# Kernel tuning notes

Measured on AMD Instinct MI355X. Metric: run time of the kernel, lower is better.

## Reference

```python
import jax, jax.numpy as jnp
import numpy as np

BS, C, H, W = 128, 256, 9, 9
D = 9                      # spectral window size
PS = 15                    # padsize
PAD_SPACE = PS - H         # 6
PAD1 = D // 2              # 4 (spectral pad)
START = PAD_SPACE // 2     # 3 (output crop offset)
SPE_HEAD = 25
SHARE_HEAD = 9
SIDE = 5                   # spe_head_Sidelength
BN_EPS = 1e-5


def setup_inputs() -> dict:
    key = jax.random.key(0)
    ks = jax.random.split(key, 12)
    s = 0.1
    return {
        "x": jax.random.normal(ks[0], (BS, C, H, W), jnp.float32),
        "wk": jax.random.normal(ks[1], (H * W, 1, D), jnp.float32) * s,   # depthwise conv1d over spectral axis
        "bk": jax.random.normal(ks[2], (H * W,), jnp.float32) * s,
        "w1": jax.random.normal(ks[3], (SPE_HEAD, SHARE_HEAD, 2 * SHARE_HEAD), jnp.float32) * s,  # grouped 1x1, no bias
        "bn_gamma": jnp.ones((SPE_HEAD * SHARE_HEAD,), jnp.float32),
        "bn_beta": jnp.zeros((SPE_HEAD * SHARE_HEAD,), jnp.float32),
        "bn_mean": jax.random.normal(ks[4], (SPE_HEAD * SHARE_HEAD,), jnp.float32) * s,
        "bn_var": jax.random.uniform(ks[5], (SPE_HEAD * SHARE_HEAD,), jnp.float32, 0.5, 1.5),
        "w2": jax.random.normal(ks[6], (SPE_HEAD, D, SHARE_HEAD), jnp.float32) * s,  # grouped 1x1 -> spe_head*d
        "b2": jax.random.normal(ks[7], (SPE_HEAD * D,), jnp.float32) * s,
        "wv": jax.random.normal(ks[8], (C, 1, 3, 3), jnp.float32) * s,   # depthwise 3x3
        "bv": jax.random.normal(ks[9], (C,), jnp.float32) * s,
    }


def _unfold_k3_d5(t, bs, c):
    # torch nn.Unfold(kernel=3, dilation=5) on a 15x15 map -> 5x5 output positions.
    # row = kh*5 + oh, col = kw*5 + ow, so a plain (3,5,3,5) reshape gives the taps.
    t = t.reshape(bs, c, 3, SIDE, 3, SIDE)              # (bs,c,kh,oh,kw,ow)
    t = t.transpose(0, 1, 2, 4, 3, 5)                   # (bs,c,kh,kw,oh,ow)
    t = t.reshape(bs, c * SHARE_HEAD, SPE_HEAD)          # (bs, c*9, 25) torch unfold layout
    return t.transpose(0, 2, 1)                          # (bs, 25, c*9)


def reference(x, wk, bk, w1, bn_gamma, bn_beta, bn_mean, bn_var, w2, b2, wv, bv):
    bs, c, h, w = x.shape
    # --- key: depthwise conv1d along spectral (channel) axis, one filter per pixel ---
    k = x.reshape(bs, c, h * w).transpose(0, 2, 1)       # (bs, 81, c)
    k1 = jax.lax.conv_general_dilated(
        k, wk, (1,), [(PAD1, PAD1)],
        dimension_numbers=("NCH", "OIH", "NCH"), feature_group_count=h * w,
    ) + bk[None, :, None]                                # (bs, 81, c)
    k1 = k1.transpose(0, 2, 1).reshape(bs, c, h, w)

    # --- pad right/bottom and unfold q, k ---
    k1_pad = jnp.pad(k1, ((0, 0), (0, 0), (0, PAD_SPACE), (0, PAD_SPACE)))  # (bs,c,15,15)
    q_pad = jnp.pad(x, ((0, 0), (0, 0), (0, PAD_SPACE), (0, PAD_SPACE)))
    key_u = _unfold_k3_d5(k1_pad, bs, c)                 # (bs,25,9c)
    q_u = _unfold_k3_d5(q_pad, bs, c)

    # stack + reshape exactly as torch (row-major): (bs,25,2,9c) -> (bs,450,c)
    key_q = jnp.stack((q_u, key_u), axis=2).reshape(bs, 2 * SPE_HEAD * SHARE_HEAD, c)

    # --- attention_embed: grouped 1x1 conv -> BN(eval) -> ReLU -> grouped 1x1 conv ---
    a = jnp.einsum("goi,bgic->bgoc", w1, key_q.reshape(bs, SPE_HEAD, 2 * SHARE_HEAD, c))
    a = a.reshape(bs, SPE_HEAD * SHARE_HEAD, c)          # (bs,225,c)
    inv_std = bn_gamma / jnp.sqrt(bn_var + BN_EPS)
    a = (a - bn_mean[None, :, None]) * inv_std[None, :, None] + bn_beta[None, :, None]
    a = jax.nn.relu(a)
    a = jnp.einsum("goi,bgic->bgoc", w2, a.reshape(bs, SPE_HEAD, SHARE_HEAD, c))
    a = a.reshape(bs, SPE_HEAD * D, c) + b2[None, :, None]  # (bs,225,c)

    # --- build per-pixel spectral kernels: tile, rearrange to 15x15, softmax over d ---
    att = jnp.tile(a.reshape(bs, SPE_HEAD, D, c), (1, SHARE_HEAD, 1, 1))  # (bs,225,9,c)
    att = att.transpose(0, 3, 1, 2)                      # (bs,c,225,d)
    att = att.reshape(bs, c, 3, 3, SIDE, SIDE, D)
    att = att.transpose(0, 1, 2, 4, 3, 5, 6)             # swap dims 3,4 as torch .transpose(3,4)
    att = att.reshape(bs, c, PS, PS, D)
    att = jax.nn.softmax(att, axis=-1)
    att = att.transpose(0, 1, 4, 2, 3)                   # (bs,c,d,15,15)

    # --- value: depthwise 3x3 conv, pad left/top + spectral, sliding window over channels ---
    v = jax.lax.conv_general_dilated(
        x, wv, (1, 1), [(1, 1), (1, 1)],
        dimension_numbers=("NCHW", "OIHW", "NCHW"), feature_group_count=c,
    ) + bv[None, :, None, None]                          # (bs,c,9,9)
    pv = jnp.pad(v, ((0, 0), (PAD1, PAD1), (PAD_SPACE, 0), (PAD_SPACE, 0)))  # (bs,c+8,15,15)
    v_unf = jnp.stack([pv[:, t:t + c] for t in range(D)], axis=2)            # (bs,c,d,15,15)

    out = jnp.sum(v_unf * att, axis=2) + k1_pad          # (bs,c,15,15)
    return out[:, :, START:h + START, START:w + START]    # (bs,c,9,9)
```

## Files before the change

kernel.cpp:

```cpp
#include <hip/hip_runtime.h>

#define C 256
#define HW 81
#define PITCH 292
#define PITCHD 146
#define ZROW 81

__device__ __forceinline__ float lo_f(unsigned int d) {
  union { unsigned int i; float f; } c; c.i = d << 16; return c.f;
}
__device__ __forceinline__ float hi_f(unsigned int d) {
  union { unsigned int i; float f; } c; c.i = d & 0xffff0000u; return c.f;
}
__device__ __forceinline__ float bf2f(unsigned short u) {
  union { unsigned int i; float f; } c; c.i = ((unsigned int)u) << 16; return c.f;
}
__device__ __forceinline__ unsigned short f2bf(float f) {
  union { float f; unsigned int i; } c; c.f = f;
  return (unsigned short)((c.i + 0x7fffu + ((c.i >> 16) & 1u)) >> 16);
}
__device__ __forceinline__ unsigned int pack2(float a, float b) {
  return (unsigned int)f2bf(a) | ((unsigned int)f2bf(b) << 16);
}

__global__ __launch_bounds__(1024) void semca_fused(
    const float* __restrict__ x, const float* __restrict__ wk,
    const float* __restrict__ bk, const float* __restrict__ w1,
    const float* __restrict__ gamma, const float* __restrict__ beta,
    const float* __restrict__ mean, const float* __restrict__ var,
    const float* __restrict__ w2, const float* __restrict__ b2,
    const float* __restrict__ wv, const float* __restrict__ bv,
    float* __restrict__ out) {
  __shared__ unsigned short xT[82 * PITCH];
  __shared__ unsigned short k1T[82 * PITCH];
  __shared__ unsigned short vT[18 * PITCH];
  __shared__ unsigned short pixtab[228];
  __shared__ float2 bnf[225];

  const int blk = blockIdx.x;
  const int b = (blk & 7) * 16 + ((blk >> 3) & 15);
  const int s = blk >> 7;
  const int tid = threadIdx.x;
  const float* xb = x + (size_t)b * (C * HW);

  unsigned int* xTd = (unsigned int*)xT;
  unsigned int* k1Td = (unsigned int*)k1T;
  unsigned int* vTd = (unsigned int*)vT;

  {
    auto stage = [&](int f) {
      int chp = f / HW;
      int p = f - chp * HW;
      xTd[PITCHD * p + 2 + chp] =
          pack2(xb[(2 * chp) * HW + p], xb[(2 * chp + 1) * HW + p]);
    };
#pragma unroll
    for (int rep = 0; rep < 10; ++rep) stage(tid + rep * 1024);
    if (tid < 128) stage(10240 + tid);
  }
  for (int t = tid; t < 810; t += 1024) {
    int p = t / 10, k2 = t - (t / 10) * 10;
    xT[p * PITCH + ((k2 < 4) ? k2 : (256 + k2))] = 0;
  }
  if (tid < PITCHD) {
    xTd[PITCHD * ZROW + tid] = 0;
    k1Td[PITCHD * ZROW + tid] = 0;
  }
  for (int t = tid; t < 225; t += 1024) {
    int g = t / 9, tap = t - (t / 9) * 9;
    int kh = tap / 3, kw = tap - kh * 3;
    int h = kh * 5 + g / 5, w = kw * 5 + (g - (g / 5) * 5);
    pixtab[t] = (h < 9 && w < 9) ? (unsigned short)((h * 9 + w) * PITCH)
                                 : (unsigned short)(ZROW * PITCH);
    float inv = gamma[t] * rsqrtf(var[t] + 1e-5f);
    bnf[t] = make_float2(inv, beta[t] - mean[t] * inv);
  }

  const int chv = tid & 127;
  float wv_e[9], wv_o[9];
#pragma unroll
  for (int t = 0; t < 9; ++t) {
    wv_e[t] = wv[(2 * chv) * 9 + t];
    wv_o[t] = wv[(2 * chv + 1) * 9 + t];
  }
  const float bv_e = bv[2 * chv], bv_o = bv[2 * chv + 1];

  __syncthreads();

  {
    auto k1fn = [&](int f) {
      int p = __builtin_amdgcn_readfirstlane(f >> 6);
      int u = f & 63;
      const uint2* wrow2 = (const uint2*)(xTd + PITCHD * p);
      uint2 q0 = wrow2[u], q1 = wrow2[u + 1], q2 = wrow2[u + 2];
      float e[12] = {lo_f(q0.x), hi_f(q0.x), lo_f(q0.y), hi_f(q0.y),
                     lo_f(q1.x), hi_f(q1.x), lo_f(q1.y), hi_f(q1.y),
                     lo_f(q2.x), hi_f(q2.x), lo_f(q2.y), hi_f(q2.y)};
      const float* wkp = wk + p * 9;
      float bkp = bk[p];
      float c0 = bkp, c1 = bkp, c2 = bkp, c3 = bkp;
#pragma unroll
      for (int j = 0; j < 9; ++j) {
        float wj = wkp[j];
        c0 = fmaf(wj, e[j], c0);
        c1 = fmaf(wj, e[j + 1], c1);
        c2 = fmaf(wj, e[j + 2], c2);
        c3 = fmaf(wj, e[j + 3], c3);
      }
      *(uint2*)(k1Td + PITCHD * p + 2 + 2 * u) =
          make_uint2(pack2(c0, c1), pack2(c2, c3));
    };
#pragma unroll
    for (int rep = 0; rep < 5; ++rep) k1fn(tid + rep * 1024);
    if (tid < 64) k1fn(5120 + tid);
  }

  {
    auto vfn = [&](int f) {
      int e = __builtin_amdgcn_readfirstlane(f >> 7);
      int r0 = e / 6;
      int i = s * 3 + r0;
      int j = e - r0 * 6;
      float a_e = bv_e, a_o = bv_o;
#pragma unroll
      for (int di = 0; di < 3; ++di) {
        int ii = i + di - 1;
        if (ii < 0) continue;
#pragma unroll
        for (int dj = 0; dj < 3; ++dj) {
          int jj = j + dj - 1;
          if (jj < 0) continue;
          unsigned int d = xTd[PITCHD * (ii * 9 + jj) + 2 + chv];
          int t = di * 3 + dj;
          a_e = fmaf(lo_f(d), wv_e[t], a_e);
          a_o = fmaf(hi_f(d), wv_o[t], a_o);
        }
      }
      vTd[PITCHD * e + 2 + chv] = pack2(a_e, a_o);
    };
#pragma unroll
    for (int rep = 0; rep < 2; ++rep) vfn(tid + rep * 1024);
    if (tid < 256) vfn(2048 + tid);
  }
  if (tid < 180) {
    int e = tid / 10, k2 = tid - (tid / 10) * 10;
    vT[e * PITCH + ((k2 < 4) ? k2 : (256 + k2))] = 0;
  }
  __syncthreads();

  const int s4 = tid >> 8;
  const int ch = tid & 255;
  const int ci0 = ch / 9;
  const int tap0 = ch - ci0 * 9;
  float* outb = out + ((size_t)b * C + ch) * HW;

  int tq[9], cq[9];
  {
    int ci = ci0, tap = tap0;
#pragma unroll
    for (int q = 0; q < 9; ++q) {
      tq[q] = tap;
      cq[q] = 4 + ci;
      tap += 4;
      ci += 28;
      if (tap >= 9) { tap -= 9; ci += 1; }
    }
  }

#define PV_STORE(OH, OW)                                                   \
  do {                                                                     \
    int e_ = gh_i * 6 + ((OW)-3);                                          \
    const unsigned short* vrow_ = vT + e_ * PITCH;                         \
    float acc_ = 0.f;                                                      \
    _Pragma("unroll") for (int d_ = 0; d_ < 9; ++d_) acc_ =                \
        fmaf(a2[d_], bf2f(vrow_[ch + d_]), acc_);                          \
    acc_ *= inv_s;                                                         \
    if ((OH) < 6 && (OW) < 6)                                              \
      acc_ += bf2f(k1T[(((OH) + 3) * 9 + ((OW) + 3)) * PITCH + 4 + ch]);   \
    if (valid_inst) outb[(OH)*9 + (OW)] = acc_;                            \
  } while (0)

#pragma unroll
  for (int k = 0; k < 4; ++k) {
    int idx = s4 * 4 + k;
    const bool valid_inst = (idx < 15);
    if (!valid_inst) idx = 14;
    int gh_i = idx / 5, gw_i = idx - (idx / 5) * 5;
    int oh = (s ? 6 : 3) + gh_i;
    int gh = s ? ((gh_i + 4) % 5) : (gh_i + 1);
    int g9 = __builtin_amdgcn_readfirstlane((gh * 5 + gw_i) * 9);

    float kq[18];
#pragma unroll
    for (int q = 0; q < 9; ++q) {
      int off = (int)pixtab[g9 + tq[q]] + cq[q];
      kq[q] = bf2f(xT[off]);
      kq[9 + q] = bf2f(k1T[off]);
    }

    __builtin_amdgcn_s_setprio(1);
    float r[9];
#pragma unroll
    for (int o = 0; o < 9; ++o) {
      int m = g9 + o;
      const float* w1m = w1 + m * 18;
      float a = 0.f;
#pragma unroll
      for (int i2 = 0; i2 < 18; ++i2) a = fmaf(w1m[i2], kq[i2], a);
      float2 bn = bnf[m];
      a = fmaf(a, bn.x, bn.y);
      r[o] = fmaxf(a, 0.f);
    }

    float a2[9], mx = -1e30f;
#pragma unroll
    for (int d = 0; d < 9; ++d) {
      int m = g9 + d;
      const float* w2m = w2 + m * 9;
      float a = b2[m];
#pragma unroll
      for (int o = 0; o < 9; ++o) a = fmaf(w2m[o], r[o], a);
      a2[d] = a;
      mx = fmaxf(mx, a);
    }
    float ssum = 0.f;
#pragma unroll
    for (int d = 0; d < 9; ++d) {
      a2[d] = __expf(a2[d] - mx);
      ssum += a2[d];
    }
    float inv_s = __builtin_amdgcn_rcpf(ssum);
    __builtin_amdgcn_s_setprio(0);

    int ow0 = (gw_i == 0) ? 7 : (gw_i + 2);
    PV_STORE(oh, ow0);
    if (gw_i == 1) PV_STORE(oh, 8);
  }
#undef PV_STORE

  if (s == 0) {
    if (s4 < 3) {
      int oh = s4;
#pragma unroll
      for (int ow = 0; ow < 9; ++ow) {
        float v2 = 0.f;
        if (ow < 6)
          v2 = bf2f(k1T[((oh + 3) * 9 + (ow + 3)) * PITCH + 4 + ch]);
        outb[oh * 9 + ow] = v2;
      }
    } else {
#pragma unroll
      for (int r0 = 0; r0 < 3; ++r0) {
        int oh = 3 + r0;
#pragma unroll
        for (int ow = 0; ow < 3; ++ow)
          outb[oh * 9 + ow] =
              bf2f(k1T[((oh + 3) * 9 + (ow + 3)) * PITCH + 4 + ch]);
      }
    }
  } else if (s4 < 3) {
    int oh = 6 + s4;
    outb[oh * 9 + 0] = 0.f;
    outb[oh * 9 + 1] = 0.f;
    outb[oh * 9 + 2] = 0.f;
  }
}

extern "C" void kernel_launch(void* const* d_in, const int* in_sizes, int n_in,
                              void* d_out, int out_size, void* d_ws, size_t ws_size,
                              hipStream_t stream) {
  const float* x     = (const float*)d_in[0];
  const float* wk    = (const float*)d_in[1];
  const float* bk    = (const float*)d_in[2];
  const float* w1    = (const float*)d_in[3];
  const float* gamma = (const float*)d_in[4];
  const float* beta  = (const float*)d_in[5];
  const float* mean  = (const float*)d_in[6];
  const float* var   = (const float*)d_in[7];
  const float* w2    = (const float*)d_in[8];
  const float* b2    = (const float*)d_in[9];
  const float* wv    = (const float*)d_in[10];
  const float* bv    = (const float*)d_in[11];
  float* out = (float*)d_out;

  hipLaunchKernelGGL(semca_fused, dim3(256), dim3(1024), 0, stream,
                     x, wk, bk, w1, gamma, beta, mean, var, w2, b2, wv, bv, out);
}
```

Measured before the change: 27.73 us.

## Interleave x and k1 in one shared array and prefetch gathers across iterations

Merges the separate bf16 x and k1 shared-memory arrays into one 32-bit-per-element array with x in the low half and k1 in the high half. The attention-kernel gather then needs one LDS load per tap instead of two. Staging and the value conv now work per channel rather than per channel pair, and the k1 computation uses wider uint4 loads and stores. The gathers for the next loop iteration are software-prefetched so their LDS latency overlaps the w1/w2 arithmetic. In exchange, staging issues more scalar global loads and shared-memory writes, and register pressure rises at 1024 threads per block.

```diff
diff --git a/kernel.cpp b/kernel.cpp
--- a/kernel.cpp
+++ b/kernel.cpp
@@ -2,8 +2,8 @@
 
 #define C 256
 #define HW 81
-#define PITCH 292
-#define PITCHD 146
+#define XP 268
+#define VP 270
 #define ZROW 81
 
 __device__ __forceinline__ float lo_f(unsigned int d) {
@@ -18,9 +18,6 @@
 __device__ __forceinline__ unsigned short f2bf(float f) {
   union { float f; unsigned int i; } c; c.f = f;
   return (unsigned short)((c.i + 0x7fffu + ((c.i >> 16) & 1u)) >> 16);
-}
-__device__ __forceinline__ unsigned int pack2(float a, float b) {
-  return (unsigned int)f2bf(a) | ((unsigned int)f2bf(b) << 16);
 }
 
 __global__ __launch_bounds__(1024) void semca_fused(
@@ -31,9 +28,8 @@
     const float* __restrict__ w2, const float* __restrict__ b2,
     const float* __restrict__ wv, const float* __restrict__ bv,
     float* __restrict__ out) {
-  __shared__ unsigned short xT[82 * PITCH];
-  __shared__ unsigned short k1T[82 * PITCH];
-  __shared__ unsigned short vT[18 * PITCH];
+  __shared__ unsigned int xk1[82 * XP];
+  __shared__ unsigned short vT[18 * VP];
   __shared__ unsigned short pixtab[228];
   __shared__ float2 bnf[225];
 
@@ -43,47 +39,43 @@
   const int tid = threadIdx.x;
   const float* xb = x + (size_t)b * (C * HW);
 
-  unsigned int* xTd = (unsigned int*)xT;
-  unsigned int* k1Td = (unsigned int*)k1T;
-  unsigned int* vTd = (unsigned int*)vT;
-
   {
     auto stage = [&](int f) {
-      int chp = f / HW;
-      int p = f - chp * HW;
-      xTd[PITCHD * p + 2 + chp] =
-          pack2(xb[(2 * chp) * HW + p], xb[(2 * chp + 1) * HW + p]);
+      int c = f / HW;
+      int p = f - c * HW;
+      xk1[XP * p + 4 + c] = (unsigned int)f2bf(xb[c * HW + p]);
     };
 #pragma unroll
-    for (int rep = 0; rep < 10; ++rep) stage(tid + rep * 1024);
-    if (tid < 128) stage(10240 + tid);
-  }
-  for (int t = tid; t < 810; t += 1024) {
-    int p = t / 10, k2 = t - (t / 10) * 10;
-    xT[p * PITCH + ((k2 < 4) ? k2 : (256 + k2))] = 0;
-  }
-  if (tid < PITCHD) {
-    xTd[PITCHD * ZROW + tid] = 0;
-    k1Td[PITCHD * ZROW + tid] = 0;
+    for (int rep = 0; rep < 20; ++rep) stage(tid + rep * 1024);
+    if (tid < 256) stage(20480 + tid);
+  }
+  for (int t = tid; t < 1240; t += 1024) {
+    if (t < 972) {
+      int row = t / 12, j = t - row * 12;
+      xk1[XP * row + ((j < 4) ? j : (256 + j))] = 0;
+    } else {
+      xk1[XP * ZROW + (t - 972)] = 0;
+    }
+  }
+  if (tid < 144) {
+    int e = tid >> 3, j = tid & 7;
+    vT[VP * e + ((j < 4) ? j : (256 + j))] = 0;
   }
   for (int t = tid; t < 225; t += 1024) {
     int g = t / 9, tap = t - (t / 9) * 9;
     int kh = tap / 3, kw = tap - kh * 3;
     int h = kh * 5 + g / 5, w = kw * 5 + (g - (g / 5) * 5);
-    pixtab[t] = (h < 9 && w < 9) ? (unsigned short)((h * 9 + w) * PITCH)
-                                 : (unsigned short)(ZROW * PITCH);
+    pixtab[t] = (h < 9 && w < 9) ? (unsigned short)((h * 9 + w) * XP)
+                                 : (unsigned short)(ZROW * XP);
     float inv = gamma[t] * rsqrtf(var[t] + 1e-5f);
     bnf[t] = make_float2(inv, beta[t] - mean[t] * inv);
   }
 
-  const int chv = tid & 127;
-  float wv_e[9], wv_o[9];
-#pragma unroll
-  for (int t = 0; t < 9; ++t) {
-    wv_e[t] = wv[(2 * chv) * 9 + t];
-    wv_o[t] = wv[(2 * chv + 1) * 9 + t];
-  }
-  const float bv_e = bv[2 * chv], bv_o = bv[2 * chv + 1];
+  const int chv = tid & 255;
+  float wvc[9];
+#pragma unroll
+  for (int t = 0; t < 9; ++t) wvc[t] = wv[chv * 9 + t];
+  const float bvc = bv[chv];
 
   __syncthreads();
 
@@ -91,11 +83,11 @@
     auto k1fn = [&](int f) {
       int p = __builtin_amdgcn_readfirstlane(f >> 6);
       int u = f & 63;
-      const uint2* wrow2 = (const uint2*)(xTd + PITCHD * p);
-      uint2 q0 = wrow2[u], q1 = wrow2[u + 1], q2 = wrow2[u + 2];
-      float e[12] = {lo_f(q0.x), hi_f(q0.x), lo_f(q0.y), hi_f(q0.y),
-                     lo_f(q1.x), hi_f(q1.x), lo_f(q1.y), hi_f(q1.y),
-                     lo_f(q2.x), hi_f(q2.x), lo_f(q2.y), hi_f(q2.y)};
+      const uint4* W = (const uint4*)(xk1 + XP * p + 4 * u);
+      uint4 A = W[0], B = W[1], Cq = W[2];
+      float e[12] = {lo_f(A.x), lo_f(A.y), lo_f(A.z), lo_f(A.w),
+                     lo_f(B.x), lo_f(B.y), lo_f(B.z), lo_f(B.w),
+                     lo_f(Cq.x), lo_f(Cq.y), lo_f(Cq.z), lo_f(Cq.w)};
       const float* wkp = wk + p * 9;
       float bkp = bk[p];
       float c0 = bkp, c1 = bkp, c2 = bkp, c3 = bkp;
@@ -107,8 +99,12 @@
         c2 = fmaf(wj, e[j + 2], c2);
         c3 = fmaf(wj, e[j + 3], c3);
       }
-      *(uint2*)(k1Td + PITCHD * p + 2 + 2 * u) =
-          make_uint2(pack2(c0, c1), pack2(c2, c3));
+      uint4 o;
+      o.x = (B.x & 0xffffu) | ((unsigned int)f2bf(c0) << 16);
+      o.y = (B.y & 0xffffu) | ((unsigned int)f2bf(c1) << 16);
+      o.z = (B.z & 0xffffu) | ((unsigned int)f2bf(c2) << 16);
+      o.w = (B.w & 0xffffu) | ((unsigned int)f2bf(c3) << 16);
+      *(uint4*)(xk1 + XP * p + 4 + 4 * u) = o;
     };
 #pragma unroll
     for (int rep = 0; rep < 5; ++rep) k1fn(tid + rep * 1024);
@@ -117,11 +113,11 @@
 
   {
     auto vfn = [&](int f) {
-      int e = __builtin_amdgcn_readfirstlane(f >> 7);
+      int e = __builtin_amdgcn_readfirstlane(f >> 8);
       int r0 = e / 6;
       int i = s * 3 + r0;
       int j = e - r0 * 6;
-      float a_e = bv_e, a_o = bv_o;
+      float a = bvc;
 #pragma unroll
       for (int di = 0; di < 3; ++di) {
         int ii = i + di - 1;
@@ -130,21 +126,15 @@
         for (int dj = 0; dj < 3; ++dj) {
           int jj = j + dj - 1;
           if (jj < 0) continue;
-          unsigned int d = xTd[PITCHD * (ii * 9 + jj) + 2 + chv];
-          int t = di * 3 + dj;
-          a_e = fmaf(lo_f(d), wv_e[t], a_e);
-          a_o = fmaf(hi_f(d), wv_o[t], a_o);
+          unsigned int d = xk1[XP * (ii * 9 + jj) + 4 + chv];
+          a = fmaf(lo_f(d), wvc[di * 3 + dj], a);
         }
       }
-      vTd[PITCHD * e + 2 + chv] = pack2(a_e, a_o);
+      vT[VP * e + 4 + chv] = f2bf(a);
     };
 #pragma unroll
-    for (int rep = 0; rep < 2; ++rep) vfn(tid + rep * 1024);
-    if (tid < 256) vfn(2048 + tid);
-  }
-  if (tid < 180) {
-    int e = tid / 10, k2 = tid - (tid / 10) * 10;
-    vT[e * PITCH + ((k2 < 4) ? k2 : (256 + k2))] = 0;
+    for (int rep = 0; rep < 4; ++rep) vfn(tid + rep * 1024);
+    if (tid < 512) vfn(4096 + tid);
   }
   __syncthreads();
 
@@ -167,36 +157,50 @@
     }
   }
 
+  int g9s[4], ohs[4], ghis[4], gwis[4];
+  bool valids[4];
+#pragma unroll
+  for (int k = 0; k < 4; ++k) {
+    int idx = s4 * 4 + k;
+    valids[k] = (idx < 15);
+    if (idx >= 15) idx = 14;
+    int gh_i = idx / 5, gw_i = idx - (idx / 5) * 5;
+    ghis[k] = gh_i;
+    gwis[k] = gw_i;
+    ohs[k] = (s ? 6 : 3) + gh_i;
+    int gh = s ? ((gh_i + 4) % 5) : (gh_i + 1);
+    g9s[k] = __builtin_amdgcn_readfirstlane((gh * 5 + gw_i) * 9);
+  }
+
 #define PV_STORE(OH, OW)                                                   \
   do {                                                                     \
     int e_ = gh_i * 6 + ((OW)-3);                                          \
-    const unsigned short* vrow_ = vT + e_ * PITCH;                         \
+    const unsigned short* vrow_ = vT + e_ * VP;                            \
     float acc_ = 0.f;                                                      \
     _Pragma("unroll") for (int d_ = 0; d_ < 9; ++d_) acc_ =                \
         fmaf(a2[d_], bf2f(vrow_[ch + d_]), acc_);                          \
     acc_ *= inv_s;                                                         \
     if ((OH) < 6 && (OW) < 6)                                              \
-      acc_ += bf2f(k1T[(((OH) + 3) * 9 + ((OW) + 3)) * PITCH + 4 + ch]);   \
+      acc_ += hi_f(xk1[XP * (((OH) + 3) * 9 + ((OW) + 3)) + 4 + ch]);      \
     if (valid_inst) outb[(OH)*9 + (OW)] = acc_;                            \
   } while (0)
 
+  unsigned int ga[9];
+#pragma unroll
+  for (int q = 0; q < 9; ++q)
+    ga[q] = xk1[(int)pixtab[g9s[0] + tq[q]] + cq[q]];
+
 #pragma unroll
   for (int k = 0; k < 4; ++k) {
-    int idx = s4 * 4 + k;
-    const bool valid_inst = (idx < 15);
-    if (!valid_inst) idx = 14;
-    int gh_i = idx / 5, gw_i = idx - (idx / 5) * 5;
-    int oh = (s ? 6 : 3) + gh_i;
-    int gh = s ? ((gh_i + 4) % 5) : (gh_i + 1);
-    int g9 = __builtin_amdgcn_readfirstlane((gh * 5 + gw_i) * 9);
-
-    float kq[18];
-#pragma unroll
-    for (int q = 0; q < 9; ++q) {
-      int off = (int)pixtab[g9 + tq[q]] + cq[q];
-      kq[q] = bf2f(xT[off]);
-      kq[9 + q] = bf2f(k1T[off]);
-    }
+    unsigned int gb[9];
+    if (k < 3) {
+#pragma unroll
+      for (int q = 0; q < 9; ++q)
+        gb[q] = xk1[(int)pixtab[g9s[k + 1] + tq[q]] + cq[q]];
+    }
+    const bool valid_inst = valids[k];
+    const int g9 = g9s[k];
+    const int gh_i = ghis[k], gw_i = gwis[k], oh = ohs[k];
 
     __builtin_amdgcn_s_setprio(1);
     float r[9];
@@ -206,7 +210,10 @@
       const float* w1m = w1 + m * 18;
       float a = 0.f;
 #pragma unroll
-      for (int i2 = 0; i2 < 18; ++i2) a = fmaf(w1m[i2], kq[i2], a);
+      for (int q = 0; q < 9; ++q) {
+        a = fmaf(w1m[q], lo_f(ga[q]), a);
+        a = fmaf(w1m[9 + q], hi_f(ga[q]), a);
+      }
       float2 bn = bnf[m];
       a = fmaf(a, bn.x, bn.y);
       r[o] = fmaxf(a, 0.f);
@@ -235,6 +242,11 @@
     int ow0 = (gw_i == 0) ? 7 : (gw_i + 2);
     PV_STORE(oh, ow0);
     if (gw_i == 1) PV_STORE(oh, 8);
+
+    if (k < 3) {
+#pragma unroll
+      for (int q = 0; q < 9; ++q) ga[q] = gb[q];
+    }
   }
 #undef PV_STORE
 
@@ -245,7 +257,7 @@
       for (int ow = 0; ow < 9; ++ow) {
         float v2 = 0.f;
         if (ow < 6)
-          v2 = bf2f(k1T[((oh + 3) * 9 + (ow + 3)) * PITCH + 4 + ch]);
+          v2 = hi_f(xk1[XP * ((oh + 3) * 9 + (ow + 3)) + 4 + ch]);
         outb[oh * 9 + ow] = v2;
       }
     } else {
@@ -255,7 +267,7 @@
 #pragma unroll
         for (int ow = 0; ow < 3; ++ow)
           outb[oh * 9 + ow] =
-              bf2f(k1T[((oh + 3) * 9 + (ow + 3)) * PITCH + 4 + ch]);
+              hi_f(xk1[XP * ((oh + 3) * 9 + (ow + 3)) + 4 + ch]);
       }
     }
   } else if (s4 < 3) {
```

Result: slower. 29.06 us (+4.8%).
